# Performance work log

Hardware: AMD Instinct MI355X
Metric: run time of the kernel (lower is better)

Reference implementation:

```python
import jax, jax.numpy as jnp
import numpy as np
import math

D_MODEL, N_HEADS, D_HEAD = 1024, 16, 64
INIT_RANGE = 0.02
IGNORE = -100000.0


def setup_inputs() -> dict:
    key = jax.random.key(0)
    ks = jax.random.split(key, 5)
    x = jax.random.normal(ks[0], (2, 2048, D_MODEL), dtype=jnp.float32)
    W_Q = INIT_RANGE * jax.random.normal(ks[1], (N_HEADS, D_MODEL, D_HEAD), dtype=jnp.float32)
    W_K = INIT_RANGE * jax.random.normal(ks[2], (N_HEADS, D_MODEL, D_HEAD), dtype=jnp.float32)
    W_V = INIT_RANGE * jax.random.normal(ks[3], (N_HEADS, D_MODEL, D_HEAD), dtype=jnp.float32)
    # W_O is contracted as 'n_heads d_head d_model' in the original einsum
    W_O = INIT_RANGE * jax.random.normal(ks[4], (N_HEADS, D_HEAD, D_MODEL), dtype=jnp.float32)
    b_Q = jnp.zeros((N_HEADS, D_HEAD), dtype=jnp.float32)
    b_K = jnp.zeros((N_HEADS, D_HEAD), dtype=jnp.float32)
    b_V = jnp.zeros((N_HEADS, D_HEAD), dtype=jnp.float32)
    b_O = jnp.zeros((D_MODEL,), dtype=jnp.float32)
    return {"normalized_resid_pre": x, "W_Q": W_Q, "b_Q": b_Q, "W_K": W_K, "b_K": b_K,
            "W_V": W_V, "b_V": b_V, "W_O": W_O, "b_O": b_O}


def reference(normalized_resid_pre, W_Q, b_Q, W_K, b_K, W_V, b_V, W_O, b_O):
    x = normalized_resid_pre  # [b, s, d_model]
    q = jnp.einsum('bsd,hde->bshe', x, W_Q) + b_Q  # [b, s, h, d_head]
    k = jnp.einsum('bsd,hde->bshe', x, W_K) + b_K
    v = jnp.einsum('bsd,hde->bshe', x, W_V) + b_V
    scores = jnp.einsum('bqhe,bkhe->bhqk', q, k) / math.sqrt(D_HEAD)
    S = x.shape[1]
    causal = jnp.tril(jnp.ones((S, S), dtype=bool))  # True where allowed
    scores = jnp.where(causal, scores, IGNORE)
    pattern = jax.nn.softmax(scores, axis=-1)  # [b, h, q, k]
    z = jnp.einsum('bhqk,bkhe->bqhe', pattern, v)
    attn_out = jnp.einsum('bqhe,hed->bqd', z, W_O) + b_O
    return attn_out
```

## Files before the change

kernel.cpp:

```cpp
#include <hip/hip_runtime.h>
#include <cstdint>
#include <cstddef>

typedef unsigned short u16;
typedef __bf16 bf16x8 __attribute__((ext_vector_type(8)));
typedef _Float16 f16x4 __attribute__((ext_vector_type(4)));
typedef _Float16 f16x2 __attribute__((ext_vector_type(2)));
typedef float  f32x4  __attribute__((ext_vector_type(4)));
typedef unsigned short u16x8 __attribute__((ext_vector_type(8)));
typedef unsigned short u16x4 __attribute__((ext_vector_type(4)));

#define DM   1024
#define NH   16
#define DH   64
#define SS   2048
#define BSZ  4096
#define NQKV 3072
#define QSCALE 0.18033688011f

__device__ __forceinline__ u16 f2b(float f) {
  unsigned u = __builtin_bit_cast(unsigned, f);
  return (u16)((u + 0x7FFFu + ((u >> 16) & 1u)) >> 16);
}
__device__ __forceinline__ u16 f2h(float f) {
  _Float16 h = (_Float16)f;
  return __builtin_bit_cast(u16, h);
}

__device__ __forceinline__ void gl_lds16(const void* g, void* l) {
  __builtin_amdgcn_global_load_lds(
      (__attribute__((address_space(1))) void*)(void*)g,
      (__attribute__((address_space(3))) void*)l, 16, 0, 0);
}

__global__ __launch_bounds__(256) void prep_all_kernel(
    const float* __restrict__ x, u16* __restrict__ xb,
    const float* __restrict__ Wq, const float* __restrict__ Wk,
    const float* __restrict__ Wv, u16* __restrict__ wqkvt,
    const float* __restrict__ Wo, u16* __restrict__ wot) {
  __shared__ __align__(16) u16 Ts[64 * 72];
  int bid = blockIdx.x, t = threadIdx.x;
  if (bid < 2048) {
    int i = (bid * 256 + t) * 8;
    float4 a = *(const float4*)(x + i);
    float4 b = *(const float4*)(x + i + 4);
    u16x8 o;
    o[0] = f2b(a.x); o[1] = f2b(a.y); o[2] = f2b(a.z); o[3] = f2b(a.w);
    o[4] = f2b(b.x); o[5] = f2b(b.y); o[6] = f2b(b.z); o[7] = f2b(b.w);
    *(u16x8*)(xb + i) = o;
    return;
  }
  if (bid < 2816) {
    int idx = bid - 2048;
    int dt = idx & 15, sl = idx >> 4;
    int proj = sl >> 4, h = sl & 15;
    const float* W = (proj == 0) ? Wq : ((proj == 1) ? Wk : Wv);
    int d0 = dt * 64;
    {
      int ld = t >> 2;
      int ec = (t & 3) * 16;
      const float* src = W + ((size_t)h * DM + d0 + ld) * DH + ec;
      float4 v0 = *(const float4*)(src);
      float4 v1 = *(const float4*)(src + 4);
      float4 v2 = *(const float4*)(src + 8);
      float4 v3 = *(const float4*)(src + 12);
      float vv[16] = {v0.x, v0.y, v0.z, v0.w, v1.x, v1.y, v1.z, v1.w,
                      v2.x, v2.y, v2.z, v2.w, v3.x, v3.y, v3.z, v3.w};
#pragma unroll
      for (int i = 0; i < 16; i++) Ts[(ec + i) * 72 + ld] = f2b(vv[i]);
    }
    __syncthreads();
    {
      int le = t >> 2;
      int dc = (t & 3) * 16;
      int n = proj * DM + h * DH + le;
      u16* dst = wqkvt + (size_t)n * DM + d0 + dc;
      *(u16x8*)(dst)     = *(const u16x8*)&Ts[le * 72 + dc];
      *(u16x8*)(dst + 8) = *(const u16x8*)&Ts[le * 72 + dc + 8];
    }
    return;
  }
  {
    int idx = bid - 2816;
    int dt = idx & 15, h = idx >> 4;
    int d0 = dt * 64;
    {
      int le = t >> 2;
      int dc = (t & 3) * 16;
      const float* src = Wo + ((size_t)h * DH + le) * DM + d0 + dc;
      float4 v0 = *(const float4*)(src);
      float4 v1 = *(const float4*)(src + 4);
      float4 v2 = *(const float4*)(src + 8);
      float4 v3 = *(const float4*)(src + 12);
      float vv[16] = {v0.x, v0.y, v0.z, v0.w, v1.x, v1.y, v1.z, v1.w,
                      v2.x, v2.y, v2.z, v2.w, v3.x, v3.y, v3.z, v3.w};
#pragma unroll
      for (int i = 0; i < 16; i++) Ts[(dc + i) * 72 + le] = f2b(vv[i]);
    }
    __syncthreads();
    {
      int ld = t >> 2;
      int ec = (t & 3) * 16;
      u16* dst = wot + (size_t)(d0 + ld) * DM + h * DH + ec;
      *(u16x8*)(dst)     = *(const u16x8*)&Ts[ld * 72 + ec];
      *(u16x8*)(dst + 8) = *(const u16x8*)&Ts[ld * 72 + ec + 8];
    }
  }
}

__global__ __launch_bounds__(256) void gemm_qkv_kernel(
    const u16* __restrict__ A, const u16* __restrict__ Bt,
    u16* __restrict__ o_q, u16* __restrict__ o_k, u16* __restrict__ o_v,
    const float* __restrict__ c0, const float* __restrict__ c1,
    const float* __restrict__ c2) {
  const int K = DM;
  __shared__ __align__(16) u16 As[128 * 32];
  __shared__ __align__(16) u16 Bs[128 * 32];
  __shared__ __align__(16) u16 Cs[64 * 128];
  int t = threadIdx.x, w = t >> 6, l = t & 63;
  int lr = l & 15, lq = l >> 4;
  int m0 = blockIdx.x * 128, n0 = blockIdx.y * 128;
  int wr = w >> 1, wc = w & 1;
  f32x4 acc[4][4] = {};
  const u16* ga = A + (size_t)(m0 + (t >> 2)) * K + (t & 3) * 8;
  const u16* gb = Bt + (size_t)(n0 + (t >> 2)) * K + (t & 3) * 8;

  for (int k0 = 0; k0 < K; k0 += 32) {
    __syncthreads();
    gl_lds16(ga + k0,           &As[w * 512]);
    gl_lds16(ga + k0 + 64 * K,  &As[2048 + w * 512]);
    gl_lds16(gb + k0,           &Bs[w * 512]);
    gl_lds16(gb + k0 + 64 * K,  &Bs[2048 + w * 512]);
    __syncthreads();
    bf16x8 af[4], bfr[4];
#pragma unroll
    for (int i = 0; i < 4; i++)
      af[i] = *(const bf16x8*)&As[(wr * 64 + i * 16 + lr) * 32 + lq * 8];
#pragma unroll
    for (int j = 0; j < 4; j++)
      bfr[j] = *(const bf16x8*)&Bs[(wc * 64 + j * 16 + lr) * 32 + lq * 8];
#pragma unroll
    for (int i = 0; i < 4; i++)
#pragma unroll
      for (int j = 0; j < 4; j++)
        acc[i][j] = __builtin_amdgcn_mfma_f32_16x16x32_bf16(af[i], bfr[j], acc[i][j], 0, 0, 0);
  }

  int proj = n0 >> 10;
  int r0 = n0 & 1023;
  int h0 = r0 >> 6;
  const float* bp = (proj == 0) ? c0 : ((proj == 1) ? c1 : c2);

#pragma unroll
  for (int p = 0; p < 2; p++) {
    __syncthreads();
    if (wr == p) {
#pragma unroll
      for (int j = 0; j < 4; j++) {
        int nl = wc * 64 + j * 16 + lr;
        float bias = bp[r0 + nl];
#pragma unroll
        for (int i = 0; i < 4; i++) {
#pragma unroll
          for (int g = 0; g < 4; g++) {
            int ml = i * 16 + lq * 4 + g;
            float val = acc[i][j][g] + bias;
            if (proj == 0)      Cs[ml * 128 + nl] = f2b(val * QSCALE);
            else if (proj == 1) Cs[ml * 128 + nl] = f2b(val);
            else                Cs[nl * 64 + ml] = f2h(val);
          }
        }
      }
    }
    __syncthreads();
    int m_base = m0 + p * 64;
    if (proj < 2) {
      int ml = t >> 2, q4 = t & 3;
      int hh = q4 >> 1, e0 = (q4 & 1) * 32;
      int m = m_base + ml, b = m >> 11, s = m & 2047;
      int h = h0 + hh;
      u16* dst = (proj == 0 ? o_q : o_k) + ((size_t)(b * NH + h) * SS + s) * DH + e0;
      const u16* src = &Cs[ml * 128 + hh * 64 + e0];
      *(u16x8*)(dst)      = *(const u16x8*)(src);
      *(u16x8*)(dst + 8)  = *(const u16x8*)(src + 8);
      *(u16x8*)(dst + 16) = *(const u16x8*)(src + 16);
      *(u16x8*)(dst + 24) = *(const u16x8*)(src + 24);
    } else {
      int er = t >> 1, sh = t & 1;
      int hh = er >> 6, e = er & 63;
      int h = h0 + hh;
      int ms = m_base + sh * 32, b = ms >> 11, s = ms & 2047;
      u16* dst = o_v + ((size_t)(b * NH + h) * DH + e) * SS + s;
      const u16* src = &Cs[er * 64 + sh * 32];
      *(u16x8*)(dst)      = *(const u16x8*)(src);
      *(u16x8*)(dst + 8)  = *(const u16x8*)(src + 8);
      *(u16x8*)(dst + 16) = *(const u16x8*)(src + 16);
      *(u16x8*)(dst + 24) = *(const u16x8*)(src + 24);
    }
  }
}

__global__ __launch_bounds__(256) void gemm_o_kernel(
    const u16* __restrict__ A, const u16* __restrict__ Bt,
    const float* __restrict__ bo, float* __restrict__ fout) {
  const int K = DM;
  __shared__ __align__(16) u16 As[128 * 32];
  __shared__ __align__(16) u16 Bs[64 * 32];
  int t = threadIdx.x, w = t >> 6, l = t & 63;
  int lr = l & 15, lq = l >> 4;
  int m0 = blockIdx.x * 128, n0 = blockIdx.y * 64;
  f32x4 acc[2][4] = {};
  const u16* ga = A + (size_t)(m0 + (t >> 2)) * K + (t & 3) * 8;
  const u16* gb = Bt + (size_t)(n0 + (t >> 2)) * K + (t & 3) * 8;

  for (int k0 = 0; k0 < K; k0 += 32) {
    __syncthreads();
    gl_lds16(ga + k0,           &As[w * 512]);
    gl_lds16(ga + k0 + 64 * K,  &As[2048 + w * 512]);
    gl_lds16(gb + k0, &Bs[w * 512]);
    __syncthreads();
    bf16x8 af[2], bfr[4];
#pragma unroll
    for (int i = 0; i < 2; i++)
      af[i] = *(const bf16x8*)&As[(w * 32 + i * 16 + lr) * 32 + lq * 8];
#pragma unroll
    for (int j = 0; j < 4; j++)
      bfr[j] = *(const bf16x8*)&Bs[(j * 16 + lr) * 32 + lq * 8];
#pragma unroll
    for (int i = 0; i < 2; i++)
#pragma unroll
      for (int j = 0; j < 4; j++)
        acc[i][j] = __builtin_amdgcn_mfma_f32_16x16x32_bf16(af[i], bfr[j], acc[i][j], 0, 0, 0);
  }

  int mb = m0 + w * 32 + lq * 4;
  int nb = n0 + lr;
#pragma unroll
  for (int j = 0; j < 4; j++) {
    int n = nb + j * 16;
    float bias = bo[n];
#pragma unroll
    for (int i = 0; i < 2; i++) {
#pragma unroll
      for (int g = 0; g < 4; g++) {
        int m = mb + i * 16 + g;
        fout[(size_t)m * DM + n] = acc[i][j][g] + bias;
      }
    }
  }
}

__global__ __launch_bounds__(128) void attn_kernel(const u16* __restrict__ q_ws,
                                                   const u16* __restrict__ k_ws,
                                                   const u16* __restrict__ vt_ws,
                                                   u16* __restrict__ z_ws) {
  __shared__ __align__(16) u16 Ks[2][64 * 72], Vs[2][64 * 72];

  int t = threadIdx.x;
  int w = t >> 6;
  int l = t & 63;
  int lr = l & 15, lq = l >> 4;
  int srow = t >> 3;
  int sc8 = (t & 7) * 8;

  int bid = blockIdx.x;
  int xcd = bid & 7, idx = bid >> 3;
  int bh = xcd * 4 + (idx & 3);
  int p = idx >> 2;
  int bq = p & 7, quad = p >> 3;
  int qt = (quad == 0) ? bq : (quad == 1) ? (15 - bq)
         : (quad == 2) ? (16 + bq) : (31 - bq);
  const u16* Qb = q_ws + (size_t)bh * SS * DH;
  const u16* Kb = k_ws + (size_t)bh * SS * DH;
  const u16* Vb = vt_ws + (size_t)bh * DH * SS;
  int b = bh >> 4, h16 = bh & 15;

  int q0 = qt * 64;
  int nkt = qt + 1;

  int qr0 = q0 + w * 32 + lr;
  bf16x8 qf00 = *(const bf16x8*)(Qb + (size_t)qr0 * DH + lq * 8);
  bf16x8 qf01 = *(const bf16x8*)(Qb + (size_t)qr0 * DH + 32 + lq * 8);
  bf16x8 qf10 = *(const bf16x8*)(Qb + (size_t)(qr0 + 16) * DH + lq * 8);
  bf16x8 qf11 = *(const bf16x8*)(Qb + (size_t)(qr0 + 16) * DH + 32 + lq * 8);

  f32x4 accO0[4] = {}, accO1[4] = {};
  float accL0 = 0.f, accL1 = 0.f;

  {
    const u16* kg = Kb + (size_t)srow * DH + sc8;
    const u16* vg = Vb + (size_t)srow * SS + sc8;
#pragma unroll
    for (int j2 = 0; j2 < 4; j2++) {
      *(u16x8*)&Ks[0][(srow + 16 * j2) * 72 + sc8] = *(const u16x8*)(kg + 16 * j2 * DH);
      *(u16x8*)&Vs[0][(srow + 16 * j2) * 72 + sc8] = *(const u16x8*)(vg + (size_t)16 * j2 * SS);
    }
  }

  for (int it = 0; it < nkt; ++it) {
    __syncthreads();
    int pb = it & 1;
    bool have_next = (it + 1 < nkt);

    u16x8 rk[4], rv[4];
    if (have_next) {
      int k0n = (it + 1) * 64;
      const u16* kg = Kb + (size_t)(k0n + srow) * DH + sc8;
      const u16* vg = Vb + (size_t)srow * SS + k0n + sc8;
#pragma unroll
      for (int j2 = 0; j2 < 4; j2++) {
        rk[j2] = *(const u16x8*)(kg + 16 * j2 * DH);
        rv[j2] = *(const u16x8*)(vg + (size_t)16 * j2 * SS);
      }
    }

    f32x4 sc0[4], sc1[4];
#pragma unroll
    for (int nt = 0; nt < 4; nt++) {
      bf16x8 kf0 = *(const bf16x8*)&Ks[pb][(nt * 16 + lr) * 72 + lq * 8];
      bf16x8 kf1 = *(const bf16x8*)&Ks[pb][(nt * 16 + lr) * 72 + 32 + lq * 8];
      f32x4 a = {0.f, 0.f, 0.f, 0.f};
      a = __builtin_amdgcn_mfma_f32_16x16x32_bf16(kf0, qf00, a, 0, 0, 0);
      a = __builtin_amdgcn_mfma_f32_16x16x32_bf16(kf1, qf01, a, 0, 0, 0);
      sc0[nt] = a;
      f32x4 c = {0.f, 0.f, 0.f, 0.f};
      c = __builtin_amdgcn_mfma_f32_16x16x32_bf16(kf0, qf10, c, 0, 0, 0);
      c = __builtin_amdgcn_mfma_f32_16x16x32_bf16(kf1, qf11, c, 0, 0, 0);
      sc1[nt] = c;
    }

    if (it == nkt - 1) {
      int k0 = it * 64;
#pragma unroll
      for (int nt = 0; nt < 4; nt++) {
#pragma unroll
        for (int gg = 0; gg < 4; gg++) {
          int gk = k0 + nt * 16 + lq * 4 + gg;
          if (gk > qr0) sc0[nt][gg] = -1e30f;
          if (gk > qr0 + 16) sc1[nt][gg] = -1e30f;
        }
      }
    }

    f16x4 pf0[4], pf1[4];
#pragma unroll
    for (int nt = 0; nt < 4; nt++) {
      float a0 = __builtin_amdgcn_exp2f(sc0[nt][0]);
      float a1 = __builtin_amdgcn_exp2f(sc0[nt][1]);
      float a2 = __builtin_amdgcn_exp2f(sc0[nt][2]);
      float a3 = __builtin_amdgcn_exp2f(sc0[nt][3]);
      accL0 += (a0 + a1) + (a2 + a3);
      f16x2 e0 = __builtin_bit_cast(f16x2, __builtin_amdgcn_cvt_pkrtz(a0, a1));
      f16x2 e1 = __builtin_bit_cast(f16x2, __builtin_amdgcn_cvt_pkrtz(a2, a3));
      pf0[nt][0] = e0[0]; pf0[nt][1] = e0[1];
      pf0[nt][2] = e1[0]; pf0[nt][3] = e1[1];
      float c0v = __builtin_amdgcn_exp2f(sc1[nt][0]);
      float c1v = __builtin_amdgcn_exp2f(sc1[nt][1]);
      float c2v = __builtin_amdgcn_exp2f(sc1[nt][2]);
      float c3v = __builtin_amdgcn_exp2f(sc1[nt][3]);
      accL1 += (c0v + c1v) + (c2v + c3v);
      f16x2 e2 = __builtin_bit_cast(f16x2, __builtin_amdgcn_cvt_pkrtz(c0v, c1v));
      f16x2 e3 = __builtin_bit_cast(f16x2, __builtin_amdgcn_cvt_pkrtz(c2v, c3v));
      pf1[nt][0] = e2[0]; pf1[nt][1] = e2[1];
      pf1[nt][2] = e3[0]; pf1[nt][3] = e3[1];
    }

#pragma unroll
    for (int ks = 0; ks < 4; ks++) {
#pragma unroll
      for (int et = 0; et < 4; et++) {
        f16x4 vf = *(const f16x4*)&Vs[pb][(et * 16 + lr) * 72 + ks * 16 + lq * 4];
        accO0[et] = __builtin_amdgcn_mfma_f32_16x16x16f16(vf, pf0[ks], accO0[et], 0, 0, 0);
        accO1[et] = __builtin_amdgcn_mfma_f32_16x16x16f16(vf, pf1[ks], accO1[et], 0, 0, 0);
      }
    }

    if (have_next) {
      int nb = (it + 1) & 1;
#pragma unroll
      for (int j2 = 0; j2 < 4; j2++) {
        *(u16x8*)&Ks[nb][(srow + 16 * j2) * 72 + sc8] = rk[j2];
        *(u16x8*)&Vs[nb][(srow + 16 * j2) * 72 + sc8] = rv[j2];
      }
    }
  }

  accL0 += __shfl_xor(accL0, 16, 64);
  accL0 += __shfl_xor(accL0, 32, 64);
  accL1 += __shfl_xor(accL1, 16, 64);
  accL1 += __shfl_xor(accL1, 32, 64);
  float inv0 = 1.0f / accL0;
  float inv1 = 1.0f / accL1;

  u16* zrow0 = z_ws + ((size_t)(b * SS + qr0)) * DM + h16 * DH;
  u16* zrow1 = z_ws + ((size_t)(b * SS + qr0 + 16)) * DM + h16 * DH;
#pragma unroll
  for (int et = 0; et < 4; et++) {
    u16x4 o0, o1;
#pragma unroll
    for (int gg = 0; gg < 4; gg++) {
      o0[gg] = f2b(accO0[et][gg] * inv0);
      o1[gg] = f2b(accO1[et][gg] * inv1);
    }
    *(u16x4*)(zrow0 + et * 16 + lq * 4) = o0;
    *(u16x4*)(zrow1 + et * 16 + lq * 4) = o1;
  }
}

extern "C" void kernel_launch(void* const* d_in, const int* in_sizes, int n_in,
                              void* d_out, int out_size, void* d_ws, size_t ws_size,
                              hipStream_t stream) {
  const float* x  = (const float*)d_in[0];
  const float* Wq = (const float*)d_in[1];
  const float* bq = (const float*)d_in[2];
  const float* Wk = (const float*)d_in[3];
  const float* bk = (const float*)d_in[4];
  const float* Wv = (const float*)d_in[5];
  const float* bv = (const float*)d_in[6];
  const float* Wo = (const float*)d_in[7];
  const float* bo = (const float*)d_in[8];
  float* out = (float*)d_out;

  char* ws = (char*)d_ws;
  const size_t MB = 1u << 20;
  u16* xb    = (u16*)(ws);
  u16* wqkvt = (u16*)(ws + 8 * MB);
  u16* wot   = (u16*)(ws + 14 * MB);
  u16* q_ws  = (u16*)(ws + 16 * MB);
  u16* k_ws  = (u16*)(ws + 24 * MB);
  u16* vt_ws = (u16*)(ws + 32 * MB);
  u16* z_ws  = (u16*)(ws + 40 * MB);

  prep_all_kernel<<<3072, 256, 0, stream>>>(x, xb, Wq, Wk, Wv, wqkvt, Wo, wot);

  gemm_qkv_kernel<<<dim3(BSZ / 128, NQKV / 128), 256, 0, stream>>>(
      xb, wqkvt, q_ws, k_ws, vt_ws, bq, bk, bv);

  attn_kernel<<<1024, 128, 0, stream>>>(q_ws, k_ws, vt_ws, z_ws);

  gemm_o_kernel<<<dim3(BSZ / 128, DM / 64), 256, 0, stream>>>(z_ws, wot, bo, out);
}
```

Measured before the change: 186.4 us.

## Swizzle GEMM LDS tiles and read attention K/V directly from global

The QKV and output-projection GEMMs now apply an XOR swizzle to the column offsets used when writing tiles into LDS and when reading them back, so fragment reads avoid LDS bank conflicts. The attention kernel drops its double-buffered K/V shared-memory staging and block barriers. Each wave instead loads its K and V MFMA fragments straight from global memory through the caches. The MFMA sections are wrapped in s_setprio raises. This removes LDS traffic and synchronisation in attention at the cost of redundant global/L2 reads (both waves fetch the same K/V) and exposed load latency with no software prefetch.

```diff
diff --git a/kernel.cpp b/kernel.cpp
--- a/kernel.cpp
+++ b/kernel.cpp
@@ -122,8 +122,10 @@
   int m0 = blockIdx.x * 128, n0 = blockIdx.y * 128;
   int wr = w >> 1, wc = w & 1;
   f32x4 acc[4][4] = {};
-  const u16* ga = A + (size_t)(m0 + (t >> 2)) * K + (t & 3) * 8;
-  const u16* gb = Bt + (size_t)(n0 + (t >> 2)) * K + (t & 3) * 8;
+  int ssw = (((t & 3) ^ ((t >> 3) & 3)) * 8);
+  const u16* ga = A + (size_t)(m0 + (t >> 2)) * K + ssw;
+  const u16* gb = Bt + (size_t)(n0 + (t >> 2)) * K + ssw;
+  int csw = (lq * 8) ^ (((lr >> 1) & 3) * 8);
 
   for (int k0 = 0; k0 < K; k0 += 32) {
     __syncthreads();
@@ -135,10 +137,10 @@
     bf16x8 af[4], bfr[4];
 #pragma unroll
     for (int i = 0; i < 4; i++)
-      af[i] = *(const bf16x8*)&As[(wr * 64 + i * 16 + lr) * 32 + lq * 8];
+      af[i] = *(const bf16x8*)&As[(wr * 64 + i * 16 + lr) * 32 + csw];
 #pragma unroll
     for (int j = 0; j < 4; j++)
-      bfr[j] = *(const bf16x8*)&Bs[(wc * 64 + j * 16 + lr) * 32 + lq * 8];
+      bfr[j] = *(const bf16x8*)&Bs[(wc * 64 + j * 16 + lr) * 32 + csw];
 #pragma unroll
     for (int i = 0; i < 4; i++)
 #pragma unroll
@@ -210,8 +212,10 @@
   int lr = l & 15, lq = l >> 4;
   int m0 = blockIdx.x * 128, n0 = blockIdx.y * 64;
   f32x4 acc[2][4] = {};
-  const u16* ga = A + (size_t)(m0 + (t >> 2)) * K + (t & 3) * 8;
-  const u16* gb = Bt + (size_t)(n0 + (t >> 2)) * K + (t & 3) * 8;
+  int ssw = (((t & 3) ^ ((t >> 3) & 3)) * 8);
+  const u16* ga = A + (size_t)(m0 + (t >> 2)) * K + ssw;
+  const u16* gb = Bt + (size_t)(n0 + (t >> 2)) * K + ssw;
+  int csw = (lq * 8) ^ (((lr >> 1) & 3) * 8);
 
   for (int k0 = 0; k0 < K; k0 += 32) {
     __syncthreads();
@@ -222,10 +226,10 @@
     bf16x8 af[2], bfr[4];
 #pragma unroll
     for (int i = 0; i < 2; i++)
-      af[i] = *(const bf16x8*)&As[(w * 32 + i * 16 + lr) * 32 + lq * 8];
+      af[i] = *(const bf16x8*)&As[(w * 32 + i * 16 + lr) * 32 + csw];
 #pragma unroll
     for (int j = 0; j < 4; j++)
-      bfr[j] = *(const bf16x8*)&Bs[(j * 16 + lr) * 32 + lq * 8];
+      bfr[j] = *(const bf16x8*)&Bs[(j * 16 + lr) * 32 + csw];
 #pragma unroll
     for (int i = 0; i < 2; i++)
 #pragma unroll
@@ -254,14 +258,10 @@
                                                    const u16* __restrict__ k_ws,
                                                    const u16* __restrict__ vt_ws,
                                                    u16* __restrict__ z_ws) {
-  __shared__ __align__(16) u16 Ks[2][64 * 72], Vs[2][64 * 72];
-
   int t = threadIdx.x;
   int w = t >> 6;
   int l = t & 63;
   int lr = l & 15, lq = l >> 4;
-  int srow = t >> 3;
-  int sc8 = (t & 7) * 8;
 
   int bid = blockIdx.x;
   int xcd = bid & 7, idx = bid >> 3;
@@ -287,50 +287,32 @@
   f32x4 accO0[4] = {}, accO1[4] = {};
   float accL0 = 0.f, accL1 = 0.f;
 
-  {
-    const u16* kg = Kb + (size_t)srow * DH + sc8;
-    const u16* vg = Vb + (size_t)srow * SS + sc8;
-#pragma unroll
-    for (int j2 = 0; j2 < 4; j2++) {
-      *(u16x8*)&Ks[0][(srow + 16 * j2) * 72 + sc8] = *(const u16x8*)(kg + 16 * j2 * DH);
-      *(u16x8*)&Vs[0][(srow + 16 * j2) * 72 + sc8] = *(const u16x8*)(vg + (size_t)16 * j2 * SS);
-    }
-  }
-
   for (int it = 0; it < nkt; ++it) {
-    __syncthreads();
-    int pb = it & 1;
-    bool have_next = (it + 1 < nkt);
-
-    u16x8 rk[4], rv[4];
-    if (have_next) {
-      int k0n = (it + 1) * 64;
-      const u16* kg = Kb + (size_t)(k0n + srow) * DH + sc8;
-      const u16* vg = Vb + (size_t)srow * SS + k0n + sc8;
-#pragma unroll
-      for (int j2 = 0; j2 < 4; j2++) {
-        rk[j2] = *(const u16x8*)(kg + 16 * j2 * DH);
-        rv[j2] = *(const u16x8*)(vg + (size_t)16 * j2 * SS);
-      }
-    }
+    int k0 = it * 64;
 
     f32x4 sc0[4], sc1[4];
+    bf16x8 kf0[4], kf1[4];
 #pragma unroll
     for (int nt = 0; nt < 4; nt++) {
-      bf16x8 kf0 = *(const bf16x8*)&Ks[pb][(nt * 16 + lr) * 72 + lq * 8];
-      bf16x8 kf1 = *(const bf16x8*)&Ks[pb][(nt * 16 + lr) * 72 + 32 + lq * 8];
+      const u16* kr = Kb + (size_t)(k0 + nt * 16 + lr) * DH;
+      kf0[nt] = *(const bf16x8*)(kr + lq * 8);
+      kf1[nt] = *(const bf16x8*)(kr + 32 + lq * 8);
+    }
+    __builtin_amdgcn_s_setprio(1);
+#pragma unroll
+    for (int nt = 0; nt < 4; nt++) {
       f32x4 a = {0.f, 0.f, 0.f, 0.f};
-      a = __builtin_amdgcn_mfma_f32_16x16x32_bf16(kf0, qf00, a, 0, 0, 0);
-      a = __builtin_amdgcn_mfma_f32_16x16x32_bf16(kf1, qf01, a, 0, 0, 0);
+      a = __builtin_amdgcn_mfma_f32_16x16x32_bf16(kf0[nt], qf00, a, 0, 0, 0);
+      a = __builtin_amdgcn_mfma_f32_16x16x32_bf16(kf1[nt], qf01, a, 0, 0, 0);
       sc0[nt] = a;
       f32x4 c = {0.f, 0.f, 0.f, 0.f};
-      c = __builtin_amdgcn_mfma_f32_16x16x32_bf16(kf0, qf10, c, 0, 0, 0);
-      c = __builtin_amdgcn_mfma_f32_16x16x32_bf16(kf1, qf11, c, 0, 0, 0);
+      c = __builtin_amdgcn_mfma_f32_16x16x32_bf16(kf0[nt], qf10, c, 0, 0, 0);
+      c = __builtin_amdgcn_mfma_f32_16x16x32_bf16(kf1[nt], qf11, c, 0, 0, 0);
       sc1[nt] = c;
     }
+    __builtin_amdgcn_s_setprio(0);
 
     if (it == nkt - 1) {
-      int k0 = it * 64;
 #pragma unroll
       for (int nt = 0; nt < 4; nt++) {
 #pragma unroll
@@ -367,21 +349,17 @@
 
 #pragma unroll
     for (int ks = 0; ks < 4; ks++) {
+      f16x4 vfr[4];
+#pragma unroll
+      for (int et = 0; et < 4; et++)
+        vfr[et] = *(const f16x4*)(Vb + (size_t)(et * 16 + lr) * SS + k0 + ks * 16 + lq * 4);
+      __builtin_amdgcn_s_setprio(1);
 #pragma unroll
       for (int et = 0; et < 4; et++) {
-        f16x4 vf = *(const f16x4*)&Vs[pb][(et * 16 + lr) * 72 + ks * 16 + lq * 4];
-        accO0[et] = __builtin_amdgcn_mfma_f32_16x16x16f16(vf, pf0[ks], accO0[et], 0, 0, 0);
-        accO1[et] = __builtin_amdgcn_mfma_f32_16x16x16f16(vf, pf1[ks], accO1[et], 0, 0, 0);
+        accO0[et] = __builtin_amdgcn_mfma_f32_16x16x16f16(vfr[et], pf0[ks], accO0[et], 0, 0, 0);
+        accO1[et] = __builtin_amdgcn_mfma_f32_16x16x16f16(vfr[et], pf1[ks], accO1[et], 0, 0, 0);
       }
-    }
-
-    if (have_next) {
-      int nb = (it + 1) & 1;
-#pragma unroll
-      for (int j2 = 0; j2 < 4; j2++) {
-        *(u16x8*)&Ks[nb][(srow + 16 * j2) * 72 + sc8] = rk[j2];
-        *(u16x8*)&Vs[nb][(srow + 16 * j2) * 72 + sc8] = rv[j2];
-      }
+      __builtin_amdgcn_s_setprio(0);
     }
   }
 
```

Measured after the change: 239.6 us. +28.5%, slower.
